# Kernel tuning notes

Hardware: AMD Instinct MI355X
Metric: run time of the kernel (lower is better)

Reference implementation:

```python
import jax, jax.numpy as jnp
import numpy as np

NEG_SLOPE = 0.2
N_NODES = 100000
N_EDGES = 1600000
IN_DIM, HIDDEN, OUT_DIM = 256, 128, 64


def _gat_conv(x, src, dst, W, a_src, a_dst, b):
    """Single-head PyG GATConv: h=xW; e_ij=LeakyReLU(a_src.h_j + a_dst.h_i);
    segment-softmax over incoming edges of each dst node; weighted scatter-add."""
    N = x.shape[0]
    h = x @ W                                   # [N, F]
    s_src = h @ a_src                           # [N]
    s_dst = h @ a_dst                           # [N]
    e = jax.nn.leaky_relu(s_src[src] + s_dst[dst], NEG_SLOPE)  # [E]
    m = jax.ops.segment_max(e, dst, num_segments=N)            # per-dst max (self-loops ensure non-empty)
    w = jnp.exp(e - m[dst])
    denom = jax.ops.segment_sum(w, dst, num_segments=N)
    alpha = w / denom[dst]                      # [E]
    out = jax.ops.segment_sum(alpha[:, None] * h[src], dst, num_segments=N)
    return out + b


def setup_inputs() -> dict:
    key = jax.random.key(0)
    ks = jax.random.split(key, 10)
    x = jax.random.normal(ks[0], (N_NODES, IN_DIM), dtype=jnp.float32)
    edge_index = jax.random.randint(ks[1], (2, N_EDGES), 0, N_NODES, dtype=jnp.int32)

    def glorot(k, shape):
        fan = sum(shape) if len(shape) > 1 else shape[0]
        return jax.random.normal(k, shape, dtype=jnp.float32) * np.sqrt(2.0 / fan)

    W1 = glorot(ks[2], (IN_DIM, HIDDEN))
    a1_src = glorot(ks[3], (HIDDEN,))
    a1_dst = glorot(ks[4], (HIDDEN,))
    b1 = jnp.zeros((HIDDEN,), dtype=jnp.float32)
    W2 = glorot(ks[5], (HIDDEN, OUT_DIM))
    a2_src = glorot(ks[6], (OUT_DIM,))
    a2_dst = glorot(ks[7], (OUT_DIM,))
    b2 = jnp.zeros((OUT_DIM,), dtype=jnp.float32)
    return {"x": x, "edge_index": edge_index, "W1": W1, "a1_src": a1_src,
            "a1_dst": a1_dst, "b1": b1, "W2": W2, "a2_src": a2_src,
            "a2_dst": a2_dst, "b2": b2}


def reference(x, edge_index, W1, a1_src, a1_dst, b1, W2, a2_src, a2_dst, b2):
    N = x.shape[0]
    loops = jnp.arange(N, dtype=edge_index.dtype)  # add_self_loops=True
    src = jnp.concatenate([edge_index[0], loops])
    dst = jnp.concatenate([edge_index[1], loops])
    h1 = jax.nn.elu(_gat_conv(x, src, dst, W1, a1_src, a1_dst, b1))  # layer 0 + ELU
    out = _gat_conv(h1, src, dst, W2, a2_src, a2_dst, b2)            # last layer, no activation
    return out
```

## Files before the change

### kernel.cpp

```cpp
#include <hip/hip_runtime.h>
#include <hip/hip_bf16.h>
#include <cstdint>
#include <cstddef>

#define NEG_SLOPE 0.2f

static __device__ __forceinline__ float leaky(float v) { return v > 0.f ? v : NEG_SLOPE * v; }
static __device__ __forceinline__ float bf_lo(unsigned r) { return __uint_as_float(r << 16); }
static __device__ __forceinline__ float bf_hi(unsigned r) { return __uint_as_float(r & 0xffff0000u); }


__global__ void hist_kernel(const int* __restrict__ dst, int E, int Etot,
                            int* __restrict__ counts) {
    int i = blockIdx.x * blockDim.x + threadIdx.x;
    if (i >= Etot) return;
    int d = (i < E) ? dst[i] : (i - E);
    atomicAdd(&counts[d], 1);
}

__global__ __launch_bounds__(256) void scan_sum_kernel(const int* __restrict__ in, int n,
                                                       int* __restrict__ bsum) {
    int base = blockIdx.x * 1024;
    int tid = threadIdx.x;
    int v = 0;
    int i0 = base + tid * 4;
    if (i0 + 3 < n) {
        int4 t4 = *reinterpret_cast<const int4*>(&in[i0]);
        v = t4.x + t4.y + t4.z + t4.w;
    } else {
        for (int q = 0; q < 4; ++q) { int i = i0 + q; if (i < n) v += in[i]; }
    }
    #pragma unroll
    for (int off = 32; off; off >>= 1) v += __shfl_xor(v, off, 64);
    __shared__ int ws[4];
    if ((tid & 63) == 0) ws[tid >> 6] = v;
    __syncthreads();
    if (tid == 0) bsum[blockIdx.x] = ws[0] + ws[1] + ws[2] + ws[3];
}

__global__ __launch_bounds__(256) void scan_mid_kernel(int* __restrict__ bsum, int nb,
                                                       int* __restrict__ totp) {
    int tid = threadIdx.x, lane = tid & 63, wid = tid >> 6;
    int v[4], run = 0;
    #pragma unroll
    for (int q = 0; q < 4; ++q) { int i = tid * 4 + q; v[q] = (i < nb) ? bsum[i] : 0; run += v[q]; }
    int x = run;
    #pragma unroll
    for (int off = 1; off < 64; off <<= 1) { int y = __shfl_up(x, off, 64); if (lane >= off) x += y; }
    __shared__ int ws[4];
    if (lane == 63) ws[wid] = x;
    __syncthreads();
    int wo = 0;
    #pragma unroll
    for (int w = 0; w < 4; ++w) if (w < wid) wo += ws[w];
    int p = wo + x - run;
    #pragma unroll
    for (int q = 0; q < 4; ++q) { int i = tid * 4 + q; if (i < nb) bsum[i] = p; p += v[q]; }
    if (tid == 255) *totp = wo + x;
}

__global__ __launch_bounds__(256) void scan_out_kernel(const int* __restrict__ in, int n,
                                                       const int* __restrict__ bsum,
                                                       int* __restrict__ out) {
    int base = blockIdx.x * 1024;
    int tid = threadIdx.x, lane = tid & 63, wid = tid >> 6;
    int v[4], run = 0;
    int i0 = base + tid * 4;
    if (i0 + 3 < n) {
        int4 t4 = *reinterpret_cast<const int4*>(&in[i0]);
        v[0] = t4.x; v[1] = t4.y; v[2] = t4.z; v[3] = t4.w;
    } else {
        for (int q = 0; q < 4; ++q) { int i = i0 + q; v[q] = (i < n) ? in[i] : 0; }
    }
    run = v[0] + v[1] + v[2] + v[3];
    int x = run;
    #pragma unroll
    for (int off = 1; off < 64; off <<= 1) { int y = __shfl_up(x, off, 64); if (lane >= off) x += y; }
    __shared__ int ws[4];
    if (lane == 63) ws[wid] = x;
    __syncthreads();
    int wo = 0;
    #pragma unroll
    for (int w = 0; w < 4; ++w) if (w < wid) wo += ws[w];
    int p = bsum[blockIdx.x] + wo + x - run;
    #pragma unroll
    for (int q = 0; q < 4; ++q) { int i = i0 + q; if (i < n) out[i] = p; p += v[q]; }
}

__global__ void fill_kernel(const int* __restrict__ src, const int* __restrict__ dst,
                            int E, int Etot, const int* __restrict__ row_start,
                            int* __restrict__ cursor, int* __restrict__ col_src) {
    int i = blockIdx.x * blockDim.x + threadIdx.x;
    if (i >= Etot) return;
    int d = (i < E) ? dst[i] : (i - E);
    int s = (i < E) ? src[i] : (i - E);
    int pos = atomicAdd(&cursor[d], 1);
    col_src[row_start[d] + pos] = s;
}


template <int NC>
__global__ __launch_bounds__(256) void gemm_kernel(const float* __restrict__ A,
                                                   const float* __restrict__ B,
                                                   __hip_bfloat16* __restrict__ C,
                                                   int M, int K) {
    constexpr int BM = 64, BK = 16;
    constexpr int TN = NC / 32;
    __shared__ float As[BK][BM + 4];
    __shared__ float Bs[BK][NC];
    int tid = threadIdx.x;
    int tx = tid & 31;
    int ty = tid >> 5;
    int m0 = blockIdx.x * BM;
    float acc[8][TN];
    #pragma unroll
    for (int r = 0; r < 8; ++r)
        #pragma unroll
        for (int c = 0; c < TN; ++c) acc[r][c] = 0.f;

    for (int k0 = 0; k0 < K; k0 += BK) {
        {
            int row = tid >> 2, kq = tid & 3;
            int gr = m0 + row;
            float4 av = (gr < M)
                ? *reinterpret_cast<const float4*>(&A[(size_t)gr * K + k0 + kq * 4])
                : make_float4(0.f, 0.f, 0.f, 0.f);
            As[kq * 4 + 0][row] = av.x;
            As[kq * 4 + 1][row] = av.y;
            As[kq * 4 + 2][row] = av.z;
            As[kq * 4 + 3][row] = av.w;
        }
        {
            constexpr int per = (BK * NC) / (256 * 4);
            #pragma unroll
            for (int pq = 0; pq < per; ++pq) {
                int idx = tid + pq * 256;
                int kr = idx / (NC / 4);
                int cc = (idx % (NC / 4)) * 4;
                float4 bv = *reinterpret_cast<const float4*>(&B[(size_t)(k0 + kr) * NC + cc]);
                *reinterpret_cast<float4*>(&Bs[kr][cc]) = bv;
            }
        }
        __syncthreads();
        #pragma unroll
        for (int k = 0; k < BK; ++k) {
            float a[8];
            float4 a0 = *reinterpret_cast<const float4*>(&As[k][ty * 8]);
            float4 a1 = *reinterpret_cast<const float4*>(&As[k][ty * 8 + 4]);
            a[0] = a0.x; a[1] = a0.y; a[2] = a0.z; a[3] = a0.w;
            a[4] = a1.x; a[5] = a1.y; a[6] = a1.z; a[7] = a1.w;
            float b[TN];
            if (TN == 4) {
                float4 bv = *reinterpret_cast<const float4*>(&Bs[k][tx * 4]);
                b[0] = bv.x; b[1] = bv.y; b[2] = bv.z; b[3] = bv.w;
            } else {
                float2 bv = *reinterpret_cast<const float2*>(&Bs[k][tx * 2]);
                b[0] = bv.x; b[1] = bv.y;
            }
            #pragma unroll
            for (int r = 0; r < 8; ++r)
                #pragma unroll
                for (int c = 0; c < TN; ++c) acc[r][c] += a[r] * b[c];
        }
        __syncthreads();
    }
    #pragma unroll
    for (int r = 0; r < 8; ++r) {
        int gr = m0 + ty * 8 + r;
        if (gr < M) {
            __hip_bfloat16 tmp[TN];
            #pragma unroll
            for (int c = 0; c < TN; ++c) tmp[c] = __float2bfloat16(acc[r][c]);
            if (TN == 4)
                *reinterpret_cast<uint2*>(&C[(size_t)gr * NC + tx * 4]) =
                    *reinterpret_cast<uint2*>(tmp);
            else
                *reinterpret_cast<unsigned*>(&C[(size_t)gr * NC + tx * 2]) =
                    *reinterpret_cast<unsigned*>(tmp);
        }
    }
}


template <int F>
__global__ __launch_bounds__(256) void score_kernel(const __hip_bfloat16* __restrict__ h,
                                                    const float* __restrict__ a_src,
                                                    const float* __restrict__ a_dst,
                                                    float* __restrict__ ss,
                                                    float* __restrict__ sd, int N) {
    int node = blockIdx.x * (blockDim.x >> 6) + (threadIdx.x >> 6);
    int lane = threadIdx.x & 63;
    if (node >= N) return;
    float vs = 0.f, vd = 0.f;
    if (F == 128) {
        unsigned r = *reinterpret_cast<const unsigned*>(&h[(size_t)node * F + lane * 2]);
        float2 asv = *reinterpret_cast<const float2*>(&a_src[lane * 2]);
        float2 adv = *reinterpret_cast<const float2*>(&a_dst[lane * 2]);
        float h0 = bf_lo(r), h1 = bf_hi(r);
        vs = h0 * asv.x + h1 * asv.y;
        vd = h0 * adv.x + h1 * adv.y;
    } else {
        unsigned r = (unsigned)*reinterpret_cast<const unsigned short*>(&h[(size_t)node * F + lane]);
        float h0 = __uint_as_float(r << 16);
        vs = h0 * a_src[lane];
        vd = h0 * a_dst[lane];
    }
    #pragma unroll
    for (int off = 32; off; off >>= 1) {
        vs += __shfl_xor(vs, off, 64);
        vd += __shfl_xor(vd, off, 64);
    }
    if (lane == 0) { ss[node] = vs; sd[node] = vd; }
}


template <int F, bool DO_ELU>
__global__ __launch_bounds__(256) void aggregate_kernel(
    const __hip_bfloat16* __restrict__ h, const float* __restrict__ ss,
    const float* __restrict__ sd, const int* __restrict__ row_start,
    const int* __restrict__ col_src, const float* __restrict__ bias,
    float* __restrict__ out, int N) {
    constexpr int EPL = F / 64;
    int node = blockIdx.x * (blockDim.x >> 6) + (threadIdx.x >> 6);
    int lane = threadIdx.x & 63;
    if (node >= N) return;
    int rs = row_start[node], re = row_start[node + 1];
    int deg = re - rs;
    float sdn = sd[node];
    float acc[EPL];
    #pragma unroll
    for (int q = 0; q < EPL; ++q) acc[q] = 0.f;

    const unsigned* h32 = reinterpret_cast<const unsigned*>(h);
    const unsigned short* h16 = reinterpret_cast<const unsigned short*>(h);

    if (deg <= 64) {
        int s_l = 0;
        float e_l = -INFINITY;
        if (lane < deg) {
            s_l = col_src[rs + lane];
            e_l = leaky(ss[s_l] + sdn);
        }
        float m = e_l;
        #pragma unroll
        for (int off = 32; off; off >>= 1) m = fmaxf(m, __shfl_xor(m, off, 64));
        float w_l = (lane < deg) ? __expf(e_l - m) : 0.f;
        float den = w_l;
        #pragma unroll
        for (int off = 32; off; off >>= 1) den += __shfl_xor(den, off, 64);
        float alpha_l = w_l / den;

        int j = 0;
        for (; j + 4 <= deg; j += 4) {
            int s0 = __shfl(s_l, j, 64), s1 = __shfl(s_l, j + 1, 64);
            int s2 = __shfl(s_l, j + 2, 64), s3 = __shfl(s_l, j + 3, 64);
            float a0 = __shfl(alpha_l, j, 64), a1 = __shfl(alpha_l, j + 1, 64);
            float a2 = __shfl(alpha_l, j + 2, 64), a3 = __shfl(alpha_l, j + 3, 64);
            if (EPL == 2) {
                unsigned r0 = h32[(size_t)s0 * (F / 2) + lane];
                unsigned r1 = h32[(size_t)s1 * (F / 2) + lane];
                unsigned r2 = h32[(size_t)s2 * (F / 2) + lane];
                unsigned r3 = h32[(size_t)s3 * (F / 2) + lane];
                acc[0] += a0 * bf_lo(r0); acc[1] += a0 * bf_hi(r0);
                acc[0] += a1 * bf_lo(r1); acc[1] += a1 * bf_hi(r1);
                acc[0] += a2 * bf_lo(r2); acc[1] += a2 * bf_hi(r2);
                acc[0] += a3 * bf_lo(r3); acc[1] += a3 * bf_hi(r3);
            } else {
                unsigned r0 = h16[(size_t)s0 * F + lane];
                unsigned r1 = h16[(size_t)s1 * F + lane];
                unsigned r2 = h16[(size_t)s2 * F + lane];
                unsigned r3 = h16[(size_t)s3 * F + lane];
                acc[0] += a0 * __uint_as_float(r0 << 16);
                acc[0] += a1 * __uint_as_float(r1 << 16);
                acc[0] += a2 * __uint_as_float(r2 << 16);
                acc[0] += a3 * __uint_as_float(r3 << 16);
            }
        }
        for (; j < deg; ++j) {
            int s0 = __shfl(s_l, j, 64);
            float a0 = __shfl(alpha_l, j, 64);
            if (EPL == 2) {
                unsigned r0 = h32[(size_t)s0 * (F / 2) + lane];
                acc[0] += a0 * bf_lo(r0); acc[1] += a0 * bf_hi(r0);
            } else {
                unsigned r0 = h16[(size_t)s0 * F + lane];
                acc[0] += a0 * __uint_as_float(r0 << 16);
            }
        }
    } else {
        float m = -INFINITY;
        for (int j = rs + lane; j < re; j += 64) {
            float e = leaky(ss[col_src[j]] + sdn);
            m = fmaxf(m, e);
        }
        #pragma unroll
        for (int off = 32; off; off >>= 1) m = fmaxf(m, __shfl_xor(m, off, 64));
        float den = 0.f;
        for (int j = rs + lane; j < re; j += 64) {
            float e = leaky(ss[col_src[j]] + sdn);
            den += __expf(e - m);
        }
        #pragma unroll
        for (int off = 32; off; off >>= 1) den += __shfl_xor(den, off, 64);
        float inv_den = 1.f / den;
        for (int j = rs; j < re; ++j) {
            int s = col_src[j];
            float e = leaky(ss[s] + sdn);
            float alpha = __expf(e - m) * inv_den;
            if (EPL == 2) {
                unsigned r0 = h32[(size_t)s * (F / 2) + lane];
                acc[0] += alpha * bf_lo(r0); acc[1] += alpha * bf_hi(r0);
            } else {
                unsigned r0 = h16[(size_t)s * F + lane];
                acc[0] += alpha * __uint_as_float(r0 << 16);
            }
        }
    }

    if (EPL == 2) {
        float2 bv = *reinterpret_cast<const float2*>(&bias[lane * 2]);
        float v0 = acc[0] + bv.x, v1 = acc[1] + bv.y;
        if (DO_ELU) {
            v0 = v0 > 0.f ? v0 : (__expf(v0) - 1.f);
            v1 = v1 > 0.f ? v1 : (__expf(v1) - 1.f);
        }
        *reinterpret_cast<float2*>(&out[(size_t)node * F + lane * 2]) = make_float2(v0, v1);
    } else {
        float v0 = acc[0] + bias[lane];
        if (DO_ELU) v0 = v0 > 0.f ? v0 : (__expf(v0) - 1.f);
        out[(size_t)node * F + lane] = v0;
    }
}


extern "C" void kernel_launch(void* const* d_in, const int* in_sizes, int n_in,
                              void* d_out, int out_size, void* d_ws, size_t ws_size,
                              hipStream_t stream) {
    const float* x   = (const float*)d_in[0];
    const int*   ei  = (const int*)d_in[1];
    const float* W1  = (const float*)d_in[2];
    const float* a1s = (const float*)d_in[3];
    const float* a1d = (const float*)d_in[4];
    const float* b1  = (const float*)d_in[5];
    const float* W2  = (const float*)d_in[6];
    const float* a2s = (const float*)d_in[7];
    const float* a2d = (const float*)d_in[8];
    const float* b2  = (const float*)d_in[9];
    float* out = (float*)d_out;

    const int N    = in_sizes[0] / 256;
    const int E    = in_sizes[1] / 2;
    const int Etot = E + N;
    const int* src = ei;
    const int* dst = ei + E;

    char* p = (char*)d_ws;
    auto carve = [&](size_t bytes) {
        char* r = p;
        p += (bytes + 255) & ~(size_t)255;
        return r;
    };
    __hip_bfloat16* h1 = (__hip_bfloat16*)carve((size_t)N * 128 * 2);
    __hip_bfloat16* h2 = (__hip_bfloat16*)carve((size_t)N * 64 * 2);
    float* x2  = (float*)carve((size_t)N * 128 * 4);
    float* s1s = (float*)carve((size_t)N * 4);
    float* s1d = (float*)carve((size_t)N * 4);
    float* s2s = (float*)carve((size_t)N * 4);
    float* s2d = (float*)carve((size_t)N * 4);
    int* counts = (int*)carve((size_t)N * 2 * 4);
    int* cursor = counts + N;
    int* row_start = (int*)carve((size_t)(N + 1) * 4);
    int* col_src   = (int*)carve((size_t)Etot * 4);
    int* bsum      = (int*)carve((size_t)2048 * 4);

    hipMemsetAsync(counts, 0, (size_t)N * 2 * 4, stream);

    const int TB = 256;
    const int nb = (N + 1023) / 1024;
    hist_kernel<<<(Etot + TB - 1) / TB, TB, 0, stream>>>(dst, E, Etot, counts);
    scan_sum_kernel<<<nb, 256, 0, stream>>>(counts, N, bsum);
    scan_mid_kernel<<<1, 256, 0, stream>>>(bsum, nb, row_start + N);
    scan_out_kernel<<<nb, 256, 0, stream>>>(counts, N, bsum, row_start);
    fill_kernel<<<(Etot + TB - 1) / TB, TB, 0, stream>>>(src, dst, E, Etot,
                                                         row_start, cursor, col_src);

    gemm_kernel<128><<<(N + 63) / 64, 256, 0, stream>>>(x, W1, h1, N, 256);
    score_kernel<128><<<(N + 3) / 4, 256, 0, stream>>>(h1, a1s, a1d, s1s, s1d, N);
    aggregate_kernel<128, true><<<(N + 3) / 4, 256, 0, stream>>>(
        h1, s1s, s1d, row_start, col_src, b1, x2, N);

    gemm_kernel<64><<<(N + 63) / 64, 256, 0, stream>>>(x2, W2, h2, N, 128);
    score_kernel<64><<<(N + 3) / 4, 256, 0, stream>>>(h2, a2s, a2d, s2s, s2d, N);
    aggregate_kernel<64, false><<<(N + 3) / 4, 256, 0, stream>>>(
        h2, s2s, s2d, row_start, col_src, b2, out, N);
}
```

Before: 587.1 us.

## Use bf16 MFMA matrix cores for both GEMMs and store hidden activations in bf16

Replaces the FP32 SIMT tiled GEMMs with MFMA 16x16x32 bf16 kernels. The first converts fp32 inputs to bf16 in registers and the second reads bf16 activations straight from global memory, with no shared memory staging. The weights are transposed and converted to bf16 by a small extra kernel each call. The layer-1 aggregate now writes bf16 output, halving the intermediate write and the second GEMM's read traffic, at the cost of lower input precision to layer 2.

```diff
diff --git a/kernel.cpp b/kernel.cpp
--- a/kernel.cpp
+++ b/kernel.cpp
@@ -5,9 +5,16 @@
 
 #define NEG_SLOPE 0.2f
 
+typedef __attribute__((ext_vector_type(8))) short short8;
+typedef __attribute__((ext_vector_type(4))) float f32x4;
+
 static __device__ __forceinline__ float leaky(float v) { return v > 0.f ? v : NEG_SLOPE * v; }
 static __device__ __forceinline__ float bf_lo(unsigned r) { return __uint_as_float(r << 16); }
 static __device__ __forceinline__ float bf_hi(unsigned r) { return __uint_as_float(r & 0xffff0000u); }
+static __device__ __forceinline__ unsigned short f2bfbits(float f) {
+    __hip_bfloat16 b = __float2bfloat16(f);
+    return *reinterpret_cast<unsigned short*>(&b);
+}
 
 
 __global__ void hist_kernel(const int* __restrict__ dst, int E, int Etot,
@@ -64,7 +71,7 @@
                                                        int* __restrict__ out) {
     int base = blockIdx.x * 1024;
     int tid = threadIdx.x, lane = tid & 63, wid = tid >> 6;
-    int v[4], run = 0;
+    int v[4];
     int i0 = base + tid * 4;
     if (i0 + 3 < n) {
         int4 t4 = *reinterpret_cast<const int4*>(&in[i0]);
@@ -72,7 +79,7 @@
     } else {
         for (int q = 0; q < 4; ++q) { int i = i0 + q; v[q] = (i < n) ? in[i] : 0; }
     }
-    run = v[0] + v[1] + v[2] + v[3];
+    int run = v[0] + v[1] + v[2] + v[3];
     int x = run;
     #pragma unroll
     for (int off = 1; off < 64; off <<= 1) { int y = __shfl_up(x, off, 64); if (lane >= off) x += y; }
@@ -99,84 +106,121 @@
 }
 
 
-template <int NC>
-__global__ __launch_bounds__(256) void gemm_kernel(const float* __restrict__ A,
-                                                   const float* __restrict__ B,
-                                                   __hip_bfloat16* __restrict__ C,
-                                                   int M, int K) {
-    constexpr int BM = 64, BK = 16;
-    constexpr int TN = NC / 32;
-    __shared__ float As[BK][BM + 4];
-    __shared__ float Bs[BK][NC];
-    int tid = threadIdx.x;
-    int tx = tid & 31;
-    int ty = tid >> 5;
-    int m0 = blockIdx.x * BM;
-    float acc[8][TN];
-    #pragma unroll
-    for (int r = 0; r < 8; ++r)
-        #pragma unroll
-        for (int c = 0; c < TN; ++c) acc[r][c] = 0.f;
-
-    for (int k0 = 0; k0 < K; k0 += BK) {
-        {
-            int row = tid >> 2, kq = tid & 3;
-            int gr = m0 + row;
-            float4 av = (gr < M)
-                ? *reinterpret_cast<const float4*>(&A[(size_t)gr * K + k0 + kq * 4])
-                : make_float4(0.f, 0.f, 0.f, 0.f);
-            As[kq * 4 + 0][row] = av.x;
-            As[kq * 4 + 1][row] = av.y;
-            As[kq * 4 + 2][row] = av.z;
-            As[kq * 4 + 3][row] = av.w;
-        }
-        {
-            constexpr int per = (BK * NC) / (256 * 4);
+__global__ void wt_kernel(const float* __restrict__ W, unsigned short* __restrict__ Wt,
+                          int K, int C) {
+    int i = blockIdx.x * blockDim.x + threadIdx.x;
+    if (i >= K * C) return;
+    int c = i / K, k = i % K;
+    Wt[i] = f2bfbits(W[(size_t)k * C + c]);
+}
+
+
+__global__ __launch_bounds__(256) void mfma_gemm1(const float* __restrict__ A,
+                                                  const unsigned short* __restrict__ Wt,
+                                                  unsigned short* __restrict__ C, int M) {
+    constexpr int K = 256, NC = 128;
+    int wave = threadIdx.x >> 6, lane = threadIdx.x & 63;
+    int lrow = lane & 15, kg = lane >> 4;
+    int m_base = blockIdx.x * 64;
+    int n0 = wave * 32;
+
+    const float* ap[4];
+    #pragma unroll
+    for (int mi = 0; mi < 4; ++mi) {
+        int row = m_base + mi * 16 + lrow;
+        if (row >= M) row = M - 1;
+        ap[mi] = A + (size_t)row * K + kg * 8;
+    }
+    const short8* bp0 = reinterpret_cast<const short8*>(Wt + (size_t)(n0 + lrow) * K + kg * 8);
+    const short8* bp1 = reinterpret_cast<const short8*>(Wt + (size_t)(n0 + 16 + lrow) * K + kg * 8);
+
+    f32x4 acc[4][2];
+    #pragma unroll
+    for (int mi = 0; mi < 4; ++mi)
+        #pragma unroll
+        for (int ni = 0; ni < 2; ++ni) acc[mi][ni] = {0.f, 0.f, 0.f, 0.f};
+
+    #pragma unroll 2
+    for (int k0 = 0; k0 < K; k0 += 32) {
+        short8 afr[4];
+        #pragma unroll
+        for (int mi = 0; mi < 4; ++mi) {
+            float4 q0 = *reinterpret_cast<const float4*>(ap[mi] + k0);
+            float4 q1 = *reinterpret_cast<const float4*>(ap[mi] + k0 + 4);
+            short8 a;
+            a[0] = (short)f2bfbits(q0.x); a[1] = (short)f2bfbits(q0.y);
+            a[2] = (short)f2bfbits(q0.z); a[3] = (short)f2bfbits(q0.w);
+            a[4] = (short)f2bfbits(q1.x); a[5] = (short)f2bfbits(q1.y);
+            a[6] = (short)f2bfbits(q1.z); a[7] = (short)f2bfbits(q1.w);
+            afr[mi] = a;
+        }
+        short8 bfr[2];
+        bfr[0] = bp0[k0 >> 3];
+        bfr[1] = bp1[k0 >> 3];
+        #pragma unroll
+        for (int mi = 0; mi < 4; ++mi)
             #pragma unroll
-            for (int pq = 0; pq < per; ++pq) {
-                int idx = tid + pq * 256;
-                int kr = idx / (NC / 4);
-                int cc = (idx % (NC / 4)) * 4;
-                float4 bv = *reinterpret_cast<const float4*>(&B[(size_t)(k0 + kr) * NC + cc]);
-                *reinterpret_cast<float4*>(&Bs[kr][cc]) = bv;
+            for (int ni = 0; ni < 2; ++ni)
+                acc[mi][ni] = __builtin_amdgcn_mfma_f32_16x16x32_bf16(afr[mi], bfr[ni],
+                                                                      acc[mi][ni], 0, 0, 0);
+    }
+
+    #pragma unroll
+    for (int mi = 0; mi < 4; ++mi) {
+        int row_b = m_base + mi * 16 + kg * 4;
+        #pragma unroll
+        for (int r = 0; r < 4; ++r) {
+            int row = row_b + r;
+            if (row < M) {
+                #pragma unroll
+                for (int ni = 0; ni < 2; ++ni)
+                    C[(size_t)row * NC + n0 + ni * 16 + lrow] = (unsigned short)f2bfbits(acc[mi][ni][r]);
             }
         }
-        __syncthreads();
-        #pragma unroll
-        for (int k = 0; k < BK; ++k) {
-            float a[8];
-            float4 a0 = *reinterpret_cast<const float4*>(&As[k][ty * 8]);
-            float4 a1 = *reinterpret_cast<const float4*>(&As[k][ty * 8 + 4]);
-            a[0] = a0.x; a[1] = a0.y; a[2] = a0.z; a[3] = a0.w;
-            a[4] = a1.x; a[5] = a1.y; a[6] = a1.z; a[7] = a1.w;
-            float b[TN];
-            if (TN == 4) {
-                float4 bv = *reinterpret_cast<const float4*>(&Bs[k][tx * 4]);
-                b[0] = bv.x; b[1] = bv.y; b[2] = bv.z; b[3] = bv.w;
-            } else {
-                float2 bv = *reinterpret_cast<const float2*>(&Bs[k][tx * 2]);
-                b[0] = bv.x; b[1] = bv.y;
-            }
-            #pragma unroll
-            for (int r = 0; r < 8; ++r)
-                #pragma unroll
-                for (int c = 0; c < TN; ++c) acc[r][c] += a[r] * b[c];
-        }
-        __syncthreads();
-    }
-    #pragma unroll
-    for (int r = 0; r < 8; ++r) {
-        int gr = m0 + ty * 8 + r;
-        if (gr < M) {
-            __hip_bfloat16 tmp[TN];
-            #pragma unroll
-            for (int c = 0; c < TN; ++c) tmp[c] = __float2bfloat16(acc[r][c]);
-            if (TN == 4)
-                *reinterpret_cast<uint2*>(&C[(size_t)gr * NC + tx * 4]) =
-                    *reinterpret_cast<uint2*>(tmp);
-            else
-                *reinterpret_cast<unsigned*>(&C[(size_t)gr * NC + tx * 2]) =
-                    *reinterpret_cast<unsigned*>(tmp);
+    }
+}
+
+
+__global__ __launch_bounds__(256) void mfma_gemm2(const unsigned short* __restrict__ A,
+                                                  const unsigned short* __restrict__ Wt,
+                                                  unsigned short* __restrict__ C, int M) {
+    constexpr int K = 128, NC = 64;
+    int wave = threadIdx.x >> 6, lane = threadIdx.x & 63;
+    int lrow = lane & 15, kg = lane >> 4;
+    int m_base = blockIdx.x * 64;
+    int n0 = wave * 16;
+
+    const short8* ap[4];
+    #pragma unroll
+    for (int mi = 0; mi < 4; ++mi) {
+        int row = m_base + mi * 16 + lrow;
+        if (row >= M) row = M - 1;
+        ap[mi] = reinterpret_cast<const short8*>(A + (size_t)row * K + kg * 8);
+    }
+    const short8* bp = reinterpret_cast<const short8*>(Wt + (size_t)(n0 + lrow) * K + kg * 8);
+
+    f32x4 acc[4];
+    #pragma unroll
+    for (int mi = 0; mi < 4; ++mi) acc[mi] = {0.f, 0.f, 0.f, 0.f};
+
+    #pragma unroll
+    for (int k0 = 0; k0 < K; k0 += 32) {
+        short8 bfr = bp[k0 >> 3];
+        #pragma unroll
+        for (int mi = 0; mi < 4; ++mi) {
+            short8 afr = ap[mi][k0 >> 3];
+            acc[mi] = __builtin_amdgcn_mfma_f32_16x16x32_bf16(afr, bfr, acc[mi], 0, 0, 0);
+        }
+    }
+
+    #pragma unroll
+    for (int mi = 0; mi < 4; ++mi) {
+        int row_b = m_base + mi * 16 + kg * 4;
+        #pragma unroll
+        for (int r = 0; r < 4; ++r) {
+            int row = row_b + r;
+            if (row < M)
+                C[(size_t)row * NC + n0 + lrow] = (unsigned short)f2bfbits(acc[mi][r]);
         }
     }
 }
@@ -214,12 +258,12 @@
 }
 
 
-template <int F, bool DO_ELU>
+template <int F, bool DO_ELU, bool OUT_BF16>
 __global__ __launch_bounds__(256) void aggregate_kernel(
     const __hip_bfloat16* __restrict__ h, const float* __restrict__ ss,
     const float* __restrict__ sd, const int* __restrict__ row_start,
     const int* __restrict__ col_src, const float* __restrict__ bias,
-    float* __restrict__ out, int N) {
+    void* __restrict__ out_raw, int N) {
     constexpr int EPL = F / 64;
     int node = blockIdx.x * (blockDim.x >> 6) + (threadIdx.x >> 6);
     int lane = threadIdx.x & 63;
@@ -324,11 +368,17 @@
             v0 = v0 > 0.f ? v0 : (__expf(v0) - 1.f);
             v1 = v1 > 0.f ? v1 : (__expf(v1) - 1.f);
         }
-        *reinterpret_cast<float2*>(&out[(size_t)node * F + lane * 2]) = make_float2(v0, v1);
+        if (OUT_BF16) {
+            unsigned pk = (unsigned)f2bfbits(v0) | ((unsigned)f2bfbits(v1) << 16);
+            reinterpret_cast<unsigned*>(out_raw)[(size_t)node * (F / 2) + lane] = pk;
+        } else {
+            reinterpret_cast<float2*>(out_raw)[(size_t)node * (F / 2) + lane] =
+                make_float2(v0, v1);
+        }
     } else {
         float v0 = acc[0] + bias[lane];
         if (DO_ELU) v0 = v0 > 0.f ? v0 : (__expf(v0) - 1.f);
-        out[(size_t)node * F + lane] = v0;
+        reinterpret_cast<float*>(out_raw)[(size_t)node * F + lane] = v0;
     }
 }
 
@@ -346,7 +396,6 @@
     const float* a2s = (const float*)d_in[7];
     const float* a2d = (const float*)d_in[8];
     const float* b2  = (const float*)d_in[9];
-    float* out = (float*)d_out;
 
     const int N    = in_sizes[0] / 256;
     const int E    = in_sizes[1] / 2;
@@ -360,9 +409,11 @@
         p += (bytes + 255) & ~(size_t)255;
         return r;
     };
-    __hip_bfloat16* h1 = (__hip_bfloat16*)carve((size_t)N * 128 * 2);
-    __hip_bfloat16* h2 = (__hip_bfloat16*)carve((size_t)N * 64 * 2);
-    float* x2  = (float*)carve((size_t)N * 128 * 4);
+    unsigned short* h1  = (unsigned short*)carve((size_t)N * 128 * 2);
+    unsigned short* h2  = (unsigned short*)carve((size_t)N * 64 * 2);
+    unsigned short* x2b = (unsigned short*)carve((size_t)N * 128 * 2);
+    unsigned short* wt1 = (unsigned short*)carve((size_t)128 * 256 * 2);
+    unsigned short* wt2 = (unsigned short*)carve((size_t)64 * 128 * 2);
     float* s1s = (float*)carve((size_t)N * 4);
     float* s1d = (float*)carve((size_t)N * 4);
     float* s2s = (float*)carve((size_t)N * 4);
@@ -377,6 +428,10 @@
 
     const int TB = 256;
     const int nb = (N + 1023) / 1024;
+
+    wt_kernel<<<(128 * 256 + TB - 1) / TB, TB, 0, stream>>>(W1, wt1, 256, 128);
+    wt_kernel<<<(64 * 128 + TB - 1) / TB, TB, 0, stream>>>(W2, wt2, 128, 64);
+
     hist_kernel<<<(Etot + TB - 1) / TB, TB, 0, stream>>>(dst, E, Etot, counts);
     scan_sum_kernel<<<nb, 256, 0, stream>>>(counts, N, bsum);
     scan_mid_kernel<<<1, 256, 0, stream>>>(bsum, nb, row_start + N);
@@ -384,13 +439,15 @@
     fill_kernel<<<(Etot + TB - 1) / TB, TB, 0, stream>>>(src, dst, E, Etot,
                                                          row_start, cursor, col_src);
 
-    gemm_kernel<128><<<(N + 63) / 64, 256, 0, stream>>>(x, W1, h1, N, 256);
-    score_kernel<128><<<(N + 3) / 4, 256, 0, stream>>>(h1, a1s, a1d, s1s, s1d, N);
-    aggregate_kernel<128, true><<<(N + 3) / 4, 256, 0, stream>>>(
-        h1, s1s, s1d, row_start, col_src, b1, x2, N);
-
-    gemm_kernel<64><<<(N + 63) / 64, 256, 0, stream>>>(x2, W2, h2, N, 128);
-    score_kernel<64><<<(N + 3) / 4, 256, 0, stream>>>(h2, a2s, a2d, s2s, s2d, N);
-    aggregate_kernel<64, false><<<(N + 3) / 4, 256, 0, stream>>>(
-        h2, s2s, s2d, row_start, col_src, b2, out, N);
-}
+    mfma_gemm1<<<(N + 63) / 64, 256, 0, stream>>>(x, wt1, h1, N);
+    score_kernel<128><<<(N + 3) / 4, 256, 0, stream>>>((const __hip_bfloat16*)h1,
+                                                       a1s, a1d, s1s, s1d, N);
+    aggregate_kernel<128, true, true><<<(N + 3) / 4, 256, 0, stream>>>(
+        (const __hip_bfloat16*)h1, s1s, s1d, row_start, col_src, b1, x2b, N);
+
+    mfma_gemm2<<<(N + 63) / 64, 256, 0, stream>>>(x2b, wt2, h2, N);
+    score_kernel<64><<<(N + 3) / 4, 256, 0, stream>>>((const __hip_bfloat16*)h2,
+                                                      a2s, a2d, s2s, s2d, N);
+    aggregate_kernel<64, false, false><<<(N + 3) / 4, 256, 0, stream>>>(
+        (const __hip_bfloat16*)h2, s2s, s2d, row_start, col_src, b2, d_out, N);
+}
```

Measured after the change: 557.0 us. 1.05x faster.
